# Kernel tuning notes

Hardware: AMD Instinct MI355X
Metric: run time of the kernel (lower is better)

## Reference

```python
import jax, jax.numpy as jnp
import numpy as np
import math

B, S, D, L, FF = 16, 2048, 512, 4, 2048
VOCAB, ATTR_VOCAB, MAXPOS = 33, 608, 2048
EPS = 1e-5


def layernorm(x, w, b):
    mu = jnp.mean(x, axis=-1, keepdims=True)
    var = jnp.mean(jnp.square(x - mu), axis=-1, keepdims=True)
    return (x - mu) * jax.lax.rsqrt(var + EPS) * w + b


def setup_inputs() -> dict:
    key = jax.random.key(0)
    ks = jax.random.split(key, 16)
    std = 0.02
    return {
        "input_ids": jax.random.randint(ks[0], (B, S), 0, VOCAB),
        "combined_indices": jax.random.randint(ks[1], (B,), 0, ATTR_VOCAB),
        "attention_mask": jnp.ones((B, S), dtype=jnp.float32),
        "tok_emb": jax.random.normal(ks[2], (VOCAB, D), jnp.float32) * std,
        "pos_emb": jax.random.normal(ks[3], (MAXPOS, D), jnp.float32) * std,
        "attr_emb": jax.random.normal(ks[4], (ATTR_VOCAB, D), jnp.float32) * std,
        "ln_w": jnp.ones((L, D), jnp.float32),
        "ln_b": jnp.zeros((L, D), jnp.float32),
        "w1": jax.random.normal(ks[5], (L, D, FF), jnp.float32) * std,
        "b1": jnp.zeros((L, FF), jnp.float32),
        "w2": jax.random.normal(ks[6], (L, FF, D), jnp.float32) * std,
        "b2": jnp.zeros((L, D), jnp.float32),
        "out_w": jax.random.normal(ks[7], (D, VOCAB), jnp.float32) * std,
        "out_b": jnp.zeros((VOCAB,), jnp.float32),
    }


def reference(input_ids, combined_indices, attention_mask, tok_emb, pos_emb,
              attr_emb, ln_w, ln_b, w1, b1, w2, b2, out_w, out_b):
    scale = 1.0 / math.sqrt(D)
    # embeddings: token + position + per-example attribute (broadcast over seq)
    x = tok_emb[input_ids] + pos_emb[jnp.arange(S)][None, :, :] \
        + attr_emb[combined_indices][:, None, :]
    mask_add = (1.0 - attention_mask)[:, None, :] * -1e9  # [B,1,S]
    for l in range(L):
        h = layernorm(x, ln_w[l], ln_b[l])                 # shared LN params used twice
        scores = jnp.einsum('bsd,btd->bst', h, h) * scale + mask_add
        probs = jax.nn.softmax(scores, axis=-1)            # dropout=0 (eval)
        attn = jnp.einsum('bst,btd->bsd', probs, h) + x    # residual
        n2 = layernorm(attn, ln_w[l], ln_b[l])
        ff = jax.nn.gelu(n2 @ w1[l] + b1[l], approximate=False) @ w2[l] + b2[l]
        x = ff + attn
    return x @ out_w + out_b
```

## Files before the change

kernel.cpp:

```cpp
#include <hip/hip_runtime.h>
#include <hip/hip_bf16.h>
#include <cmath>

#define B_ 16
#define S_ 2048
#define D_ 512
#define L_ 4
#define FF_ 2048
#define V_ 33

typedef unsigned short u16;
typedef __attribute__((ext_vector_type(8))) short bf16x8;
typedef __attribute__((ext_vector_type(4))) float f32x4;

__device__ __forceinline__ u16 f2bf(float f) {
    unsigned x = __float_as_uint(f);
    unsigned r = (x + 0x7fffu + ((x >> 16) & 1u)) >> 16;
    return (u16)r;
}
__device__ __forceinline__ float bf2f(u16 u) { return __uint_as_float(((unsigned)u) << 16); }

__device__ __forceinline__ float wave_sum(float v) {
#pragma unroll
    for (int o = 32; o; o >>= 1) v += __shfl_xor(v, o);
    return v;
}

__device__ __forceinline__ void gload16(const u16* g, u16* l) {
    __builtin_amdgcn_global_load_lds((const __attribute__((address_space(1))) void*)g,
                                     (__attribute__((address_space(3))) void*)l, 16, 0, 0);
}

__device__ __forceinline__ uint4 pack8(const u16* ov) {
    uint4 p;
    p.x = (unsigned)ov[0] | ((unsigned)ov[1] << 16);
    p.y = (unsigned)ov[2] | ((unsigned)ov[3] << 16);
    p.z = (unsigned)ov[4] | ((unsigned)ov[5] << 16);
    p.w = (unsigned)ov[6] | ((unsigned)ov[7] << 16);
    return p;
}

__global__ __launch_bounds__(256) void embed_kernel(
    const int* __restrict__ ids, const int* __restrict__ attr,
    const float* __restrict__ tok, const float* __restrict__ pos,
    const float* __restrict__ attre, float* __restrict__ x)
{
    int idx = blockIdx.x * 256 + threadIdx.x;
    const int total = B_ * S_ * (D_ / 4);
    if (idx >= total) return;
    int d4 = idx & (D_ / 4 - 1);
    int bs = idx >> 7;
    int s  = bs & (S_ - 1);
    int b  = bs >> 11;
    int id = ids[bs];
    int a  = attr[b];
    float4 t  = ((const float4*)tok)[id * (D_ / 4) + d4];
    float4 p  = ((const float4*)pos)[s * (D_ / 4) + d4];
    float4 at = ((const float4*)attre)[a * (D_ / 4) + d4];
    float4 o;
    o.x = t.x + p.x + at.x; o.y = t.y + p.y + at.y;
    o.z = t.z + p.z + at.z; o.w = t.w + p.w + at.w;
    ((float4*)x)[idx] = o;
}

__global__ __launch_bounds__(256) void ln_kernel(
    const float* __restrict__ in, u16* __restrict__ out,
    const float* __restrict__ w, const float* __restrict__ b, int rows)
{
    int gw = (int)((blockIdx.x * 256 + threadIdx.x) >> 6);
    int lane = threadIdx.x & 63;
    if (gw >= rows) return;
    const float4* p = (const float4*)(in + (size_t)gw * D_);
    float4 a0 = p[lane * 2], a1 = p[lane * 2 + 1];
    float xv[8] = {a0.x, a0.y, a0.z, a0.w, a1.x, a1.y, a1.z, a1.w};
    float s = 0.f;
#pragma unroll
    for (int k = 0; k < 8; k++) s += xv[k];
    s = wave_sum(s);
    float mu = s * (1.f / D_);
    float q = 0.f;
#pragma unroll
    for (int k = 0; k < 8; k++) { float d = xv[k] - mu; q += d * d; }
    q = wave_sum(q);
    float rs = rsqrtf(q * (1.f / D_) + 1e-5f);
    const float4* w4 = (const float4*)w;
    const float4* b4 = (const float4*)b;
    float4 w0 = w4[lane * 2], w1v = w4[lane * 2 + 1];
    float4 b0 = b4[lane * 2], b1v = b4[lane * 2 + 1];
    float wv[8] = {w0.x, w0.y, w0.z, w0.w, w1v.x, w1v.y, w1v.z, w1v.w};
    float bv[8] = {b0.x, b0.y, b0.z, b0.w, b1v.x, b1v.y, b1v.z, b1v.w};
    u16 ov[8];
#pragma unroll
    for (int k = 0; k < 8; k++) ov[k] = f2bf((xv[k] - mu) * rs * wv[k] + bv[k]);
    *(uint4*)(out + (size_t)gw * D_ + lane * 8) = pack8(ov);
}

__device__ __forceinline__ float toF(float v) { return v; }
__device__ __forceinline__ float toF(u16 v) { return bf2f(v); }

template <typename T>
__global__ void transpose_bf(const T* __restrict__ in, u16* __restrict__ out,
                             int R, int C, size_t sIn, size_t sOut)
{
    __shared__ float tile[32][33];
    const T* ip = in + (size_t)blockIdx.z * sIn;
    u16* op = out + (size_t)blockIdx.z * sOut;
    int tx = threadIdx.x, ty = threadIdx.y;
    int c = blockIdx.x * 32 + tx;
#pragma unroll
    for (int i = 0; i < 4; i++) {
        int r = blockIdx.y * 32 + ty + i * 8;
        tile[ty + i * 8][tx] = toF(ip[(size_t)r * C + c]);
    }
    __syncthreads();
#pragma unroll
    for (int i = 0; i < 4; i++) {
        int oc = blockIdx.x * 32 + ty + i * 8;
        op[(size_t)oc * R + blockIdx.y * 32 + tx] = f2bf(tile[tx][ty + i * 8]);
    }
}

__global__ __launch_bounds__(256) void rowred_kernel(
    const float* __restrict__ psum, float* __restrict__ lsum, int rows)
{
    int row = blockIdx.x * 256 + threadIdx.x;
    if (row >= rows) return;
    float s = 0.f;
#pragma unroll
    for (int i = 0; i < 32; i++) s += psum[(size_t)i * rows + row];
    lsum[row] = s;
}

enum { E_SC = 0, E_PV = 1, E_GELU = 2, E_FF2 = 3 };

template <int EPI>
__global__ __launch_bounds__(256) void gemm_nt(
    const u16* __restrict__ A, size_t sAz, int lda,
    const u16* __restrict__ B, size_t sBz, int ldb,
    float* Cf, u16* Cb, size_t sCz, int ldc,
    int K, float scale,
    const float* resid, size_t sRz,
    const float* __restrict__ bias,
    const float* __restrict__ aux, int b0,
    float* __restrict__ psum)
{
    __shared__ __align__(16) u16 ldsA[128 * 64];
    __shared__ __align__(16) u16 ldsB[128 * 64];

    const int gx = gridDim.x, gy = gridDim.y;
    const int nwg = gx * gy * gridDim.z;
    int lid = blockIdx.x + gx * (blockIdx.y + gy * blockIdx.z);
    {
        const int q = nwg >> 3, r = nwg & 7;
        const int xcd = lid & 7, idx = lid >> 3;
        lid = (xcd < r ? xcd * (q + 1) : r * (q + 1) + (xcd - r) * q) + idx;
    }
    const int bx = lid % gx;
    const int t2 = lid / gx;
    const int by = t2 % gy;
    const int z  = t2 / gy;

    A += (size_t)z * sAz;
    B += (size_t)z * sBz;
    const size_t coff = (size_t)z * sCz;
    const int brow = by * 128, bcol = bx * 128;
    const int tid = threadIdx.x, lane = tid & 63, wid = tid >> 6;
    const int wr = wid >> 1, wc = wid & 1;

    f32x4 acc[4][4];
#pragma unroll
    for (int m = 0; m < 4; m++)
#pragma unroll
        for (int n = 0; n < 4; n++) acc[m][n] = 0.0f;

    const int lg   = lane >> 3;
    const int srow = wid * 8 + lg;
    const int skk  = ((lane & 7) ^ lg) << 3;

    const int l15 = lane & 15, l7 = lane & 7, kh = lane >> 4;

    for (int k0 = 0; k0 < K; k0 += 64) {
        __syncthreads();
#pragma unroll
        for (int r = 0; r < 4; r++) {
            const u16* ga = A + (size_t)(brow + r * 32 + srow) * lda + (k0 + skk);
            const u16* gb = B + (size_t)(bcol + r * 32 + srow) * ldb + (k0 + skk);
            gload16(ga, &ldsA[r * 2048 + wid * 512]);
            gload16(gb, &ldsB[r * 2048 + wid * 512]);
        }
        __syncthreads();
#pragma unroll
        for (int kk = 0; kk < 64; kk += 32) {
            const int kc = (kk >> 3) + kh;
            const int kswz = ((kc ^ l7) << 3);
            bf16x8 af[4], bfv[4];
#pragma unroll
            for (int m = 0; m < 4; m++)
                af[m] = *(const bf16x8*)&ldsA[(wr * 64 + m * 16 + l15) * 64 + kswz];
#pragma unroll
            for (int n = 0; n < 4; n++)
                bfv[n] = *(const bf16x8*)&ldsB[(wc * 64 + n * 16 + l15) * 64 + kswz];
#pragma unroll
            for (int m = 0; m < 4; m++)
#pragma unroll
                for (int n = 0; n < 4; n++)
                    acc[m][n] = __builtin_amdgcn_mfma_f32_16x16x32_bf16(af[m], bfv[n], acc[m][n], 0, 0, 0);
        }
    }

    float rsum[4][4];
#pragma unroll
    for (int m = 0; m < 4; m++)
#pragma unroll
        for (int j = 0; j < 4; j++) rsum[m][j] = 0.f;

#pragma unroll
    for (int m = 0; m < 4; m++)
#pragma unroll
        for (int n = 0; n < 4; n++) {
            int rowb = brow + wr * 64 + m * 16 + ((lane >> 4) << 2);
            int col  = bcol + wc * 64 + n * 16 + l15;
#pragma unroll
            for (int j = 0; j < 4; j++) {
                int row = rowb + j;
                float v = acc[m][n][j];
                size_t off = coff + (size_t)row * ldc + col;
                if constexpr (EPI == E_SC) {
                    float mv = aux[(size_t)(b0 + z) * S_ + col];
                    float ev = __expf(v * scale + (1.f - mv) * -1e9f);
                    Cb[off] = f2bf(ev);
                    rsum[m][j] += ev;
                } else if constexpr (EPI == E_PV) {
                    float lv = aux[(size_t)z * S_ + row];
                    Cf[off] = v / lv + resid[(size_t)z * sRz + (size_t)row * ldc + col];
                } else if constexpr (EPI == E_GELU) {
                    float t = v + bias[col];
                    Cb[off] = f2bf(0.5f * t * (1.f + erff(t * 0.70710678118f)));
                } else {
                    Cf[off] = v + bias[col] + resid[(size_t)row * ldc + col];
                }
            }
        }

    if constexpr (EPI == E_SC) {
        const int nrows = gridDim.z * S_;
#pragma unroll
        for (int m = 0; m < 4; m++) {
            int rowl = brow + wr * 64 + m * 16 + ((lane >> 4) << 2);
#pragma unroll
            for (int j = 0; j < 4; j++) {
                float s = rsum[m][j];
                s += __shfl_xor(s, 1);
                s += __shfl_xor(s, 2);
                s += __shfl_xor(s, 4);
                s += __shfl_xor(s, 8);
                if (l15 == 0)
                    psum[(size_t)(bx * 2 + wc) * nrows + (size_t)z * S_ + rowl + j] = s;
            }
        }
    }
}

__global__ __launch_bounds__(256) void wtb_kernel(
    const float* __restrict__ W, u16* __restrict__ WTb)
{
    int i = blockIdx.x * 256 + threadIdx.x;
    if (i >= 64 * 512) return;
    int n = i >> 9, k = i & 511;
    WTb[i] = f2bf(n < V_ ? W[k * V_ + n] : 0.f);
}

__global__ __launch_bounds__(256) void outproj_mfma(
    const float* __restrict__ x, const u16* __restrict__ WTb,
    const float* __restrict__ bias, float* __restrict__ out)
{
    __shared__ __align__(16) u16 ldsA[128 * 64];
    __shared__ __align__(16) u16 ldsB[64 * 64];
    __shared__ float obuf[128][34];
    const int brow = blockIdx.x * 128;
    const int tid = threadIdx.x, lane = tid & 63, wid = tid >> 6;
    const int wr = wid >> 1, wc = wid & 1;
    const int l15 = lane & 15, l7 = lane & 7, kh = lane >> 4;
    const int lg = lane >> 3, srow = wid * 8 + lg;
    const int skk = ((lane & 7) ^ lg) << 3;
    const int ar = tid >> 1, ah = (tid & 1) * 32;

    f32x4 acc[4][2];
#pragma unroll
    for (int m = 0; m < 4; m++)
#pragma unroll
        for (int n = 0; n < 2; n++) acc[m][n] = 0.0f;

    for (int k0 = 0; k0 < 512; k0 += 64) {
        __syncthreads();
#pragma unroll
        for (int r = 0; r < 2; r++)
            gload16(WTb + (size_t)(r * 32 + srow) * 512 + (k0 + skk),
                    &ldsB[r * 2048 + wid * 512]);
        const float4* xs = (const float4*)(x + (size_t)(brow + ar) * 512 + k0 + ah);
#pragma unroll
        for (int j = 0; j < 4; j++) {
            float4 a = xs[j * 2], b = xs[j * 2 + 1];
            u16 t[8] = {f2bf(a.x), f2bf(a.y), f2bf(a.z), f2bf(a.w),
                        f2bf(b.x), f2bf(b.y), f2bf(b.z), f2bf(b.w)};
            int kc = (ah >> 3) + j;
            *(uint4*)&ldsA[ar * 64 + ((kc ^ (ar & 7)) << 3)] = pack8(t);
        }
        __syncthreads();
#pragma unroll
        for (int kk = 0; kk < 64; kk += 32) {
            const int kc = (kk >> 3) + kh;
            const int kswz = ((kc ^ l7) << 3);
            bf16x8 af[4], bfv[2];
#pragma unroll
            for (int m = 0; m < 4; m++)
                af[m] = *(const bf16x8*)&ldsA[(wr * 64 + m * 16 + l15) * 64 + kswz];
#pragma unroll
            for (int n = 0; n < 2; n++)
                bfv[n] = *(const bf16x8*)&ldsB[(wc * 32 + n * 16 + l15) * 64 + kswz];
#pragma unroll
            for (int m = 0; m < 4; m++)
#pragma unroll
                for (int n = 0; n < 2; n++)
                    acc[m][n] = __builtin_amdgcn_mfma_f32_16x16x32_bf16(af[m], bfv[n], acc[m][n], 0, 0, 0);
        }
    }

#pragma unroll
    for (int m = 0; m < 4; m++)
#pragma unroll
        for (int n = 0; n < 2; n++) {
            int rowl = wr * 64 + m * 16 + ((lane >> 4) << 2);
            int col  = wc * 32 + n * 16 + l15;
            if (col < V_) {
#pragma unroll
                for (int j = 0; j < 4; j++)
                    obuf[rowl + j][col] = acc[m][n][j] + bias[col];
            }
        }
    __syncthreads();
    float* ob = out + (size_t)brow * V_;
#pragma unroll 1
    for (int i = tid; i < 128 * V_; i += 256)
        ob[i] = obuf[i / V_][i % V_];
}

extern "C" void kernel_launch(void* const* d_in, const int* in_sizes, int n_in,
                              void* d_out, int out_size, void* d_ws, size_t ws_size,
                              hipStream_t stream)
{
    const int*   input_ids = (const int*)d_in[0];
    const int*   comb      = (const int*)d_in[1];
    const float* amask     = (const float*)d_in[2];
    const float* tok       = (const float*)d_in[3];
    const float* pos       = (const float*)d_in[4];
    const float* attre     = (const float*)d_in[5];
    const float* ln_w      = (const float*)d_in[6];
    const float* ln_b      = (const float*)d_in[7];
    const float* w1        = (const float*)d_in[8];
    const float* b1        = (const float*)d_in[9];
    const float* w2        = (const float*)d_in[10];
    const float* b2        = (const float*)d_in[11];
    const float* out_w     = (const float*)d_in[12];
    const float* out_b     = (const float*)d_in[13];
    float* out = (float*)d_out;
    (void)in_sizes; (void)n_in; (void)out_size;

    int NB_A, RC;
    if      (ws_size >= 335000000ULL) { NB_A = 16; RC = 32768; }
    else if (ws_size >= 215000000ULL) { NB_A = 8;  RC = 16384; }
    else if (ws_size >= 152000000ULL) { NB_A = 4;  RC = 8192;  }
    else                              { NB_A = 2;  RC = 4096;  }
    const int HR = NB_A * S_;

    unsigned char* ws = (unsigned char*)d_ws;
    size_t off = 0;
    auto carve = [&](size_t bytes) {
        void* p = ws + off;
        off += (bytes + 255) & ~(size_t)255;
        return p;
    };
    float* x    = (float*)carve((size_t)B_ * S_ * D_ * 4);
    u16* w1t    = (u16*)carve((size_t)L_ * D_ * FF_ * 2);
    u16* w2t    = (u16*)carve((size_t)L_ * D_ * FF_ * 2);
    u16* h      = (u16*)carve((size_t)HR * D_ * 2);
    u16* hT     = (u16*)carve((size_t)NB_A * S_ * D_ * 2);
    float* lsum = (float*)carve((size_t)NB_A * S_ * 4);
    float* psum = (float*)carve((size_t)NB_A * S_ * 32 * 4);
    u16* WTb    = (u16*)carve((size_t)64 * 512 * 2);
    size_t scP_bytes  = (size_t)NB_A * S_ * S_ * 2;
    size_t tbuf_bytes = (size_t)RC * FF_ * 2;
    void* un = carve(scP_bytes > tbuf_bytes ? scP_bytes : tbuf_bytes);
    u16* scP  = (u16*)un;
    u16* tbuf = (u16*)un;

    const float scl = 1.0f / sqrtf((float)D_);
    const int nG = B_ / NB_A;
    const int nC = (B_ * S_) / RC;

    embed_kernel<<<(B_ * S_ * (D_ / 4)) / 256, 256, 0, stream>>>(input_ids, comb, tok, pos, attre, x);
    transpose_bf<float><<<dim3(FF_ / 32, D_ / 32, L_), dim3(32, 8), 0, stream>>>(
        w1, w1t, D_, FF_, (size_t)D_ * FF_, (size_t)FF_ * D_);
    transpose_bf<float><<<dim3(D_ / 32, FF_ / 32, L_), dim3(32, 8), 0, stream>>>(
        w2, w2t, FF_, D_, (size_t)FF_ * D_, (size_t)D_ * FF_);
    wtb_kernel<<<128, 256, 0, stream>>>(out_w, WTb);

    for (int l = 0; l < L_; l++) {
        const float* lw = ln_w + l * D_;
        const float* lb = ln_b + l * D_;

        for (int g = 0; g < nG; g++) {
            float* xg = x + (size_t)g * NB_A * S_ * D_;
            ln_kernel<<<(NB_A * S_) / 4, 256, 0, stream>>>(xg, h, lw, lb, NB_A * S_);
            transpose_bf<u16><<<dim3(D_ / 32, S_ / 32, NB_A), dim3(32, 8), 0, stream>>>(
                h, hT, S_, D_, (size_t)S_ * D_, (size_t)S_ * D_);
            gemm_nt<E_SC><<<dim3(S_ / 128, S_ / 128, NB_A), 256, 0, stream>>>(
                h, (size_t)S_ * D_, D_,
                h, (size_t)S_ * D_, D_,
                nullptr, scP, (size_t)S_ * S_, S_,
                D_, scl, nullptr, 0, nullptr, amask, g * NB_A, psum);
            rowred_kernel<<<(NB_A * S_ + 255) / 256, 256, 0, stream>>>(psum, lsum, NB_A * S_);
            gemm_nt<E_PV><<<dim3(D_ / 128, S_ / 128, NB_A), 256, 0, stream>>>(
                scP, (size_t)S_ * S_, S_,
                hT, (size_t)S_ * D_, S_,
                xg, nullptr, (size_t)S_ * D_, D_,
                S_, 1.f, xg, (size_t)S_ * D_, nullptr, lsum, 0, nullptr);
        }

        for (int c = 0; c < nC; c++) {
            size_t roff = (size_t)c * RC;
            ln_kernel<<<RC / 4, 256, 0, stream>>>(x + roff * D_, h, lw, lb, RC);
            gemm_nt<E_GELU><<<dim3(FF_ / 128, RC / 128, 1), 256, 0, stream>>>(
                h, 0, D_,
                w1t + (size_t)l * FF_ * D_, 0, D_,
                nullptr, tbuf, 0, FF_,
                D_, 1.f, nullptr, 0, b1 + l * FF_, nullptr, 0, nullptr);
            gemm_nt<E_FF2><<<dim3(D_ / 128, RC / 128, 1), 256, 0, stream>>>(
                tbuf, 0, FF_,
                w2t + (size_t)l * D_ * FF_, 0, FF_,
                x + roff * D_, nullptr, 0, D_,
                FF_, 1.f, x + roff * D_, 0, b2 + l * D_, nullptr, 0, nullptr);
        }
    }

    outproj_mfma<<<(B_ * S_) / 128, 256, 0, stream>>>(x, WTb, out_b, out);
}
```

Measured before the change: 2.115 ms.

## Replace 128x128 GEMM with 256x256 eight-wave double-buffered pipelined kernel

Replaces the single-buffered 128x128 tile GEMM with a 256x256 tile, 512-thread kernel. It double-buffers LDS (128 KB) and interleaves global-to-LDS staging of the next K tiles with MFMA phases, using explicit barriers, waitcnt and setprio scheduling. The larger tile raises arithmetic intensity and the pipelining hides load latency behind compute. In exchange it uses far more LDS and registers per block, so the launch_bounds(512,2) occupancy target may not be reachable. Grids also shrink, e.g. the PV and FF2 GEMMs drop to 2 column blocks, which could leave CUs idle.

```diff
diff --git a/kernel.cpp b/kernel.cpp
--- a/kernel.cpp
+++ b/kernel.cpp
@@ -133,8 +133,35 @@
 
 enum { E_SC = 0, E_PV = 1, E_GELU = 2, E_FF2 = 3 };
 
+#define PH(BUF, Q, SSTMT, VSTMT)                                               \
+    {                                                                          \
+        if ((Q) == 0) {                                                        \
+            _Pragma("unroll") for (int n = 0; n < 4; n++)                      \
+                _Pragma("unroll") for (int ks = 0; ks < 2; ks++)               \
+                    bq[n][ks] = rdB(BUF, n, ks);                               \
+        }                                                                      \
+        bf16x8 aq[2][2];                                                       \
+        _Pragma("unroll") for (int dm = 0; dm < 2; dm++)                       \
+            _Pragma("unroll") for (int ks = 0; ks < 2; ks++)                   \
+                aq[dm][ks] = rdA(BUF, (Q) * 2 + dm, ks);                       \
+        SSTMT;                                                                 \
+        VSTMT;                                                                 \
+        __builtin_amdgcn_s_barrier();                                          \
+        asm volatile("s_waitcnt lgkmcnt(0)" ::: "memory");                     \
+        __builtin_amdgcn_sched_barrier(0);                                     \
+        __builtin_amdgcn_s_setprio(1);                                         \
+        _Pragma("unroll") for (int ks = 0; ks < 2; ks++)                       \
+            _Pragma("unroll") for (int dm = 0; dm < 2; dm++)                   \
+                _Pragma("unroll") for (int n = 0; n < 4; n++)                  \
+                    acc[(Q) * 2 + dm][n] =                                     \
+                        __builtin_amdgcn_mfma_f32_16x16x32_bf16(               \
+                            aq[dm][ks], bq[n][ks], acc[(Q) * 2 + dm][n], 0, 0, 0); \
+        __builtin_amdgcn_s_setprio(0);                                         \
+        __builtin_amdgcn_s_barrier();                                          \
+    }
+
 template <int EPI>
-__global__ __launch_bounds__(256) void gemm_nt(
+__global__ __launch_bounds__(512, 2) void gemm8p(
     const u16* __restrict__ A, size_t sAz, int lda,
     const u16* __restrict__ B, size_t sBz, int ldb,
     float* Cf, u16* Cb, size_t sCz, int ldc,
@@ -144,8 +171,7 @@
     const float* __restrict__ aux, int b0,
     float* __restrict__ psum)
 {
-    __shared__ __align__(16) u16 ldsA[128 * 64];
-    __shared__ __align__(16) u16 ldsB[128 * 64];
+    __shared__ __align__(16) u16 lds[8][8192];
 
     const int gx = gridDim.x, gy = gridDim.y;
     const int nwg = gx * gy * gridDim.z;
@@ -163,62 +189,79 @@
     A += (size_t)z * sAz;
     B += (size_t)z * sBz;
     const size_t coff = (size_t)z * sCz;
-    const int brow = by * 128, bcol = bx * 128;
+    const int brow = by * 256, bcol = bx * 256;
     const int tid = threadIdx.x, lane = tid & 63, wid = tid >> 6;
-    const int wr = wid >> 1, wc = wid & 1;
-
-    f32x4 acc[4][4];
-#pragma unroll
-    for (int m = 0; m < 4; m++)
+    const int wr = wid >> 2, wc = wid & 3;
+    const int l15 = lane & 15, l7 = lane & 7, kh = lane >> 4;
+    const int lg = lane >> 3;
+    const int skk = ((lane & 7) ^ lg) << 3;
+
+    f32x4 acc[8][4];
+#pragma unroll
+    for (int m = 0; m < 8; m++)
 #pragma unroll
         for (int n = 0; n < 4; n++) acc[m][n] = 0.0f;
 
-    const int lg   = lane >> 3;
-    const int srow = wid * 8 + lg;
-    const int skk  = ((lane & 7) ^ lg) << 3;
-
-    const int l15 = lane & 15, l7 = lane & 7, kh = lane >> 4;
-
-    for (int k0 = 0; k0 < K; k0 += 64) {
-        __syncthreads();
-#pragma unroll
-        for (int r = 0; r < 4; r++) {
-            const u16* ga = A + (size_t)(brow + r * 32 + srow) * lda + (k0 + skk);
-            const u16* gb = B + (size_t)(bcol + r * 32 + srow) * ldb + (k0 + skk);
-            gload16(ga, &ldsA[r * 2048 + wid * 512]);
-            gload16(gb, &ldsB[r * 2048 + wid * 512]);
-        }
-        __syncthreads();
-#pragma unroll
-        for (int kk = 0; kk < 64; kk += 32) {
-            const int kc = (kk >> 3) + kh;
-            const int kswz = ((kc ^ l7) << 3);
-            bf16x8 af[4], bfv[4];
-#pragma unroll
-            for (int m = 0; m < 4; m++)
-                af[m] = *(const bf16x8*)&ldsA[(wr * 64 + m * 16 + l15) * 64 + kswz];
-#pragma unroll
-            for (int n = 0; n < 4; n++)
-                bfv[n] = *(const bf16x8*)&ldsB[(wc * 64 + n * 16 + l15) * 64 + kswz];
-#pragma unroll
-            for (int m = 0; m < 4; m++)
-#pragma unroll
-                for (int n = 0; n < 4; n++)
-                    acc[m][n] = __builtin_amdgcn_mfma_f32_16x16x32_bf16(af[m], bfv[n], acc[m][n], 0, 0, 0);
-        }
-    }
-
-    float rsum[4][4];
-#pragma unroll
-    for (int m = 0; m < 4; m++)
-#pragma unroll
-        for (int j = 0; j < 4; j++) rsum[m][j] = 0.f;
-
-#pragma unroll
-    for (int m = 0; m < 4; m++)
+    auto stage = [&](int op, int buf, int half, int kt) {
+        const u16* g = (op == 0 ? A : B);
+        const int ld = (op == 0 ? lda : ldb);
+        const int rb = (op == 0 ? brow : bcol) + half * 128;
+        u16* slot = lds[buf * 4 + op * 2 + half];
+        const int kb = kt * 64 + skk;
+#pragma unroll
+        for (int r = 0; r < 2; r++)
+            gload16(g + (size_t)(rb + r * 64 + wid * 8 + lg) * ld + kb,
+                    slot + (r * 64 + wid * 8) * 64);
+    };
+    auto rdA = [&](int buf, int m, int ks) -> bf16x8 {
+        const u16* s = lds[buf * 4 + wr];
+        return *(const bf16x8*)(s + (m * 16 + l15) * 64 + (((ks * 4 + kh) ^ l7) << 3));
+    };
+    auto rdB = [&](int buf, int n, int ks) -> bf16x8 {
+        const u16* s = lds[buf * 4 + 2 + (wc >> 1)];
+        return *(const bf16x8*)(s + ((wc & 1) * 64 + n * 16 + l15) * 64 +
+                                (((ks * 4 + kh) ^ l7) << 3));
+    };
+
+    const int nit = K >> 7;
+    bf16x8 bq[4][2];
+
+    stage(0, 0, 0, 0); stage(0, 0, 1, 0);
+    stage(1, 0, 0, 0); stage(1, 0, 1, 0);
+    stage(1, 1, 0, 1); stage(1, 1, 1, 1);
+    asm volatile("s_waitcnt vmcnt(4)" ::: "memory");
+    __builtin_amdgcn_s_barrier();
+
+    for (int it = 0; it < nit; it++) {
+        const int k1 = 2 * it + 1, k2 = 2 * it + 2, k3 = 2 * it + 3;
+        const bool more = (it + 1 < nit);
+        PH(0, 0, stage(0, 1, 0, k1), (void)0);
+        PH(0, 1, stage(0, 1, 1, k1), (void)0);
+        PH(0, 2, if (more) stage(1, 0, 0, k2), (void)0);
+        PH(0, 3, if (more) stage(1, 0, 1, k2),
+                 if (more) { asm volatile("s_waitcnt vmcnt(4)" ::: "memory"); }
+                 else      { asm volatile("s_waitcnt vmcnt(0)" ::: "memory"); });
+        PH(1, 0, if (more) stage(0, 0, 0, k2), (void)0);
+        PH(1, 1, if (more) stage(0, 0, 1, k2), (void)0);
+        PH(1, 2, if (more) stage(1, 1, 0, k3), (void)0);
+        PH(1, 3, if (more) { stage(1, 1, 1, k3);
+                             asm volatile("s_waitcnt vmcnt(4)" ::: "memory"); },
+                 (void)0);
+    }
+
+    float rsum[8][4];
+    if constexpr (EPI == E_SC) {
+#pragma unroll
+        for (int m = 0; m < 8; m++)
+#pragma unroll
+            for (int j = 0; j < 4; j++) rsum[m][j] = 0.f;
+    }
+
+#pragma unroll
+    for (int m = 0; m < 8; m++)
 #pragma unroll
         for (int n = 0; n < 4; n++) {
-            int rowb = brow + wr * 64 + m * 16 + ((lane >> 4) << 2);
+            int rowb = brow + wr * 128 + m * 16 + (kh << 2);
             int col  = bcol + wc * 64 + n * 16 + l15;
 #pragma unroll
             for (int j = 0; j < 4; j++) {
@@ -245,8 +288,8 @@
     if constexpr (EPI == E_SC) {
         const int nrows = gridDim.z * S_;
 #pragma unroll
-        for (int m = 0; m < 4; m++) {
-            int rowl = brow + wr * 64 + m * 16 + ((lane >> 4) << 2);
+        for (int m = 0; m < 8; m++) {
+            int rowl = brow + wr * 128 + m * 16 + (kh << 2);
 #pragma unroll
             for (int j = 0; j < 4; j++) {
                 float s = rsum[m][j];
@@ -255,7 +298,7 @@
                 s += __shfl_xor(s, 4);
                 s += __shfl_xor(s, 8);
                 if (l15 == 0)
-                    psum[(size_t)(bx * 2 + wc) * nrows + (size_t)z * S_ + rowl + j] = s;
+                    psum[(size_t)(bx * 4 + wc) * nrows + (size_t)z * S_ + rowl + j] = s;
             }
         }
     }
@@ -414,13 +457,13 @@
             ln_kernel<<<(NB_A * S_) / 4, 256, 0, stream>>>(xg, h, lw, lb, NB_A * S_);
             transpose_bf<u16><<<dim3(D_ / 32, S_ / 32, NB_A), dim3(32, 8), 0, stream>>>(
                 h, hT, S_, D_, (size_t)S_ * D_, (size_t)S_ * D_);
-            gemm_nt<E_SC><<<dim3(S_ / 128, S_ / 128, NB_A), 256, 0, stream>>>(
+            gemm8p<E_SC><<<dim3(S_ / 256, S_ / 256, NB_A), 512, 0, stream>>>(
                 h, (size_t)S_ * D_, D_,
                 h, (size_t)S_ * D_, D_,
                 nullptr, scP, (size_t)S_ * S_, S_,
                 D_, scl, nullptr, 0, nullptr, amask, g * NB_A, psum);
             rowred_kernel<<<(NB_A * S_ + 255) / 256, 256, 0, stream>>>(psum, lsum, NB_A * S_);
-            gemm_nt<E_PV><<<dim3(D_ / 128, S_ / 128, NB_A), 256, 0, stream>>>(
+            gemm8p<E_PV><<<dim3(D_ / 256, S_ / 256, NB_A), 512, 0, stream>>>(
                 scP, (size_t)S_ * S_, S_,
                 hT, (size_t)S_ * D_, S_,
                 xg, nullptr, (size_t)S_ * D_, D_,
@@ -430,12 +473,12 @@
         for (int c = 0; c < nC; c++) {
             size_t roff = (size_t)c * RC;
             ln_kernel<<<RC / 4, 256, 0, stream>>>(x + roff * D_, h, lw, lb, RC);
-            gemm_nt<E_GELU><<<dim3(FF_ / 128, RC / 128, 1), 256, 0, stream>>>(
+            gemm8p<E_GELU><<<dim3(FF_ / 256, RC / 256, 1), 512, 0, stream>>>(
                 h, 0, D_,
                 w1t + (size_t)l * FF_ * D_, 0, D_,
                 nullptr, tbuf, 0, FF_,
                 D_, 1.f, nullptr, 0, b1 + l * FF_, nullptr, 0, nullptr);
-            gemm_nt<E_FF2><<<dim3(D_ / 128, RC / 128, 1), 256, 0, stream>>>(
+            gemm8p<E_FF2><<<dim3(D_ / 256, RC / 256, 1), 512, 0, stream>>>(
                 tbuf, 0, FF_,
                 w2t + (size_t)l * D_ * FF_, 0, FF_,
                 x + roff * D_, nullptr, 0, D_,
```

Measured after the change: 2.438 ms. 15.2% more time.
